# Kernel optimization log

Measured on AMD Instinct MI355X. Metric: run time of the kernel, lower is better.

Reference implementation:

```python
import jax, jax.numpy as jnp
import numpy as np


def setup_inputs() -> dict:
    key = jax.random.key(0)
    k1, k2 = jax.random.split(key)
    frame_t = jax.random.normal(k1, (8, 64, 256, 256), dtype=jnp.float32)
    # flow in pixel units (the module divides by W/H to normalize)
    flow_field = jax.random.normal(k2, (8, 2, 256, 256), dtype=jnp.float32) * 8.0
    return {"frame_t": frame_t, "flow_field": flow_field}


def _identity_grid(N, H, W, dtype):
    # F.affine_grid with identity theta, align_corners=False:
    # x_j = (2*(j+0.5))/W - 1, y_i = (2*(i+0.5))/H - 1
    xs = (jnp.arange(W, dtype=dtype) + 0.5) * (2.0 / W) - 1.0
    ys = (jnp.arange(H, dtype=dtype) + 0.5) * (2.0 / H) - 1.0
    gy, gx = jnp.meshgrid(ys, xs, indexing="ij")  # (H, W)
    grid = jnp.stack([gx, gy], axis=-1)  # (H, W, 2) with (x, y) last
    return jnp.broadcast_to(grid, (N, H, W, 2))


def _grid_sample_bilinear_zeros(img, grid):
    # img: (N, C, H, W); grid: (N, H, W, 2) normalized coords, align_corners=False,
    # padding_mode='zeros', mode='bilinear' (torch F.grid_sample defaults)
    N, C, H, W = img.shape
    x = grid[..., 0]
    y = grid[..., 1]
    # unnormalize (align_corners=False)
    ix = ((x + 1.0) * W - 1.0) * 0.5
    iy = ((y + 1.0) * H - 1.0) * 0.5
    ix0 = jnp.floor(ix)
    iy0 = jnp.floor(iy)
    ix1 = ix0 + 1.0
    iy1 = iy0 + 1.0
    wx1 = ix - ix0
    wx0 = 1.0 - wx1
    wy1 = iy - iy0
    wy0 = 1.0 - wy1

    b = jnp.arange(N)[:, None, None]  # (N,1,1)

    def gather(yy, xx):
        valid = (xx >= 0) & (xx <= W - 1) & (yy >= 0) & (yy <= H - 1)
        xc = jnp.clip(xx, 0, W - 1).astype(jnp.int32)
        yc = jnp.clip(yy, 0, H - 1).astype(jnp.int32)
        v = img[b, :, yc, xc]  # (N, H, W, C)
        return v * valid[..., None].astype(img.dtype)

    v00 = gather(iy0, ix0)
    v01 = gather(iy0, ix1)
    v10 = gather(iy1, ix0)
    v11 = gather(iy1, ix1)

    out = (v00 * (wy0 * wx0)[..., None]
           + v01 * (wy0 * wx1)[..., None]
           + v10 * (wy1 * wx0)[..., None]
           + v11 * (wy1 * wx1)[..., None])  # (N, H, W, C)
    return jnp.transpose(out, (0, 3, 1, 2))  # (N, C, H, W)


def reference(frame_t, flow_field):
    N, C, H, W = frame_t.shape
    std = _identity_grid(N, H, W, frame_t.dtype)  # (N, H, W, 2)
    # normalize flow by spatial size (channel 0 -> x/W, channel 1 -> y/H)
    scale = jnp.array([1.0 / W, 1.0 / H], dtype=flow_field.dtype).reshape(1, 2, 1, 1)
    flow_norm = flow_field * scale
    grid = std + jnp.transpose(flow_norm, (0, 2, 3, 1))  # (N, H, W, 2)
    return _grid_sample_bilinear_zeros(frame_t, grid)
```

## Files before the change

### kernel.cpp

```cpp
#include <hip/hip_runtime.h>


#define B_ 8
#define C_ 64
#define H_ 256
#define W_ 256
#define HW_ (H_ * W_)
#define BAND 16
#define NBAND (H_ / BAND)
#define HALO_LO 24
#define WROWS 64
#define WFLOATS (WROWS * W_)

__global__ __launch_bounds__(256, 2) void warp_bilinear_kernel(
    const float* __restrict__ frame,
    const float* __restrict__ flow,
    float* __restrict__ out)
{
    __shared__ float win[WFLOATS];

    const int blk  = blockIdx.x;
    const int b    = blk & 7;
    const int t    = blk >> 3;
    const int band = t & (NBAND - 1);
    const int c    = t >> 4;

    const int r0  = band * BAND;
    const int wlo = r0 - HALO_LO;

    const int tid = threadIdx.x;
    const float* __restrict__ src = frame + ((size_t)(b * C_ + c)) * HW_;

#pragma unroll
    for (int it = 0; it < WFLOATS / (256 * 4); ++it) {
        const int lin = it * 1024 + tid * 4;
        const int wr  = lin >> 8;
        const int wx  = lin & 255;
        const int gy  = min(max(wlo + wr, 0), H_ - 1);
        const float4 v = *(const float4*)(src + gy * W_ + wx);
        *(float4*)(win + lin) = v;
    }
    __syncthreads();

    const int px = tid;
    float* __restrict__ dst = out + ((size_t)(b * C_ + c)) * HW_;
    const float* __restrict__ flx = flow + (size_t)(b * 2 + 0) * HW_;
    const float* __restrict__ fly = flow + (size_t)(b * 2 + 1) * HW_;

    for (int r = 0; r < BAND; ++r) {
        const int py = r0 + r;
        const int sp = py * W_ + px;

        const float fx = flx[sp];
        const float fy = fly[sp];

        const float ix = (float)px + 0.5f * fx;
        const float iy = (float)py + 0.5f * fy;

        const float ix0f = floorf(ix);
        const float iy0f = floorf(iy);
        const float wx1 = ix - ix0f;
        const float wx0 = 1.0f - wx1;
        const float wy1 = iy - iy0f;
        const float wy0 = 1.0f - wy1;

        const int ix0 = (int)ix0f;
        const int iy0 = (int)iy0f;
        const int ix1 = ix0 + 1;
        const int iy1 = iy0 + 1;

        const float vx0 = (ix0 >= 0 && ix0 < W_) ? 1.0f : 0.0f;
        const float vx1 = (ix1 >= 0 && ix1 < W_) ? 1.0f : 0.0f;
        const float vy0 = (iy0 >= 0 && iy0 < H_) ? 1.0f : 0.0f;
        const float vy1 = (iy1 >= 0 && iy1 < H_) ? 1.0f : 0.0f;

        const int xc0 = min(max(ix0, 0), W_ - 1);
        const int xc1 = min(max(ix1, 0), W_ - 1);
        const int yc0 = min(max(iy0, 0), H_ - 1);
        const int yc1 = min(max(iy1, 0), H_ - 1);

        const float w00 = wy0 * wx0 * vy0 * vx0;
        const float w01 = wy0 * wx1 * vy0 * vx1;
        const float w10 = wy1 * wx0 * vy1 * vx0;
        const float w11 = wy1 * wx1 * vy1 * vx1;

        auto tap = [&](int yc, int xc) -> float {
            const int wr = yc - wlo;
            if ((unsigned)wr < (unsigned)WROWS) {
                return win[wr * W_ + xc];
            }
            return src[yc * W_ + xc];
        };

        const float t00 = tap(yc0, xc0);
        const float t01 = tap(yc0, xc1);
        const float t10 = tap(yc1, xc0);
        const float t11 = tap(yc1, xc1);

        const float v = w00 * t00 + w01 * t01 + w10 * t10 + w11 * t11;
        __builtin_nontemporal_store(v, dst + sp);
    }
}

extern "C" void kernel_launch(void* const* d_in, const int* in_sizes, int n_in,
                              void* d_out, int out_size, void* d_ws, size_t ws_size,
                              hipStream_t stream) {
    const float* frame = (const float*)d_in[0];
    const float* flow  = (const float*)d_in[1];
    float* out = (float*)d_out;

    dim3 grid(B_ * C_ * NBAND);
    dim3 block(256);
    warp_bilinear_kernel<<<grid, block, 0, stream>>>(frame, flow, out);
}
```

Baseline: 311.0 us.

## Process channel groups per block, reusing precomputed bilinear weights and offsets

```diff
diff --git a/kernel.cpp b/kernel.cpp
--- a/kernel.cpp
+++ b/kernel.cpp
@@ -8,97 +8,136 @@
 #define HW_ (H_ * W_)
 #define BAND 16
 #define NBAND (H_ / BAND)
-#define HALO_LO 24
-#define WROWS 64
-#define WFLOATS (WROWS * W_)
+#define CG 8
+#define NCG (C_ / CG)
+#define HALO 21
+#define WROWS 60
+#define WSTRIDE 260
+#define WFLOATS (WROWS * WSTRIDE)
 
 __global__ __launch_bounds__(256, 2) void warp_bilinear_kernel(
     const float* __restrict__ frame,
     const float* __restrict__ flow,
     float* __restrict__ out)
 {
-    __shared__ float win[WFLOATS];
+    __shared__ float winbuf[WFLOATS + 1];
+    float* win = winbuf + 1;
 
     const int blk  = blockIdx.x;
     const int b    = blk & 7;
     const int t    = blk >> 3;
     const int band = t & (NBAND - 1);
-    const int c    = t >> 4;
+    const int cg   = t >> 4;
 
     const int r0  = band * BAND;
-    const int wlo = r0 - HALO_LO;
+    const int wlo = r0 - HALO;
+    const int tid = threadIdx.x;
+    const int px  = tid;
 
-    const int tid = threadIdx.x;
-    const float* __restrict__ src = frame + ((size_t)(b * C_ + c)) * HW_;
-
-#pragma unroll
-    for (int it = 0; it < WFLOATS / (256 * 4); ++it) {
-        const int lin = it * 1024 + tid * 4;
-        const int wr  = lin >> 8;
-        const int wx  = lin & 255;
-        const int gy  = min(max(wlo + wr, 0), H_ - 1);
-        const float4 v = *(const float4*)(src + gy * W_ + wx);
-        *(float4*)(win + lin) = v;
-    }
-    __syncthreads();
-
-    const int px = tid;
-    float* __restrict__ dst = out + ((size_t)(b * C_ + c)) * HW_;
     const float* __restrict__ flx = flow + (size_t)(b * 2 + 0) * HW_;
     const float* __restrict__ fly = flow + (size_t)(b * 2 + 1) * HW_;
 
+    float w00[BAND], w01[BAND], w10[BAND], w11[BAND];
+    int   A0[BAND], A1[BAND];
+    unsigned wave_esc = 0u;
+
+#pragma unroll
     for (int r = 0; r < BAND; ++r) {
         const int py = r0 + r;
         const int sp = py * W_ + px;
-
         const float fx = flx[sp];
         const float fy = fly[sp];
-
         const float ix = (float)px + 0.5f * fx;
         const float iy = (float)py + 0.5f * fy;
-
         const float ix0f = floorf(ix);
         const float iy0f = floorf(iy);
-        const float wx1 = ix - ix0f;
-        const float wx0 = 1.0f - wx1;
-        const float wy1 = iy - iy0f;
-        const float wy0 = 1.0f - wy1;
-
+        const float tx = ix - ix0f;
+        const float ty = iy - iy0f;
         const int ix0 = (int)ix0f;
         const int iy0 = (int)iy0f;
         const int ix1 = ix0 + 1;
         const int iy1 = iy0 + 1;
-
-        const float vx0 = (ix0 >= 0 && ix0 < W_) ? 1.0f : 0.0f;
-        const float vx1 = (ix1 >= 0 && ix1 < W_) ? 1.0f : 0.0f;
-        const float vy0 = (iy0 >= 0 && iy0 < H_) ? 1.0f : 0.0f;
-        const float vy1 = (iy1 >= 0 && iy1 < H_) ? 1.0f : 0.0f;
-
-        const int xc0 = min(max(ix0, 0), W_ - 1);
-        const int xc1 = min(max(ix1, 0), W_ - 1);
+        const float vx0 = ((unsigned)ix0 < (unsigned)W_) ? 1.f : 0.f;
+        const float vx1 = ((unsigned)ix1 < (unsigned)W_) ? 1.f : 0.f;
+        const float vy0 = ((unsigned)iy0 < (unsigned)H_) ? 1.f : 0.f;
+        const float vy1 = ((unsigned)iy1 < (unsigned)H_) ? 1.f : 0.f;
+        w00[r] = (1.f - ty) * (1.f - tx) * vy0 * vx0;
+        w01[r] = (1.f - ty) * tx         * vy0 * vx1;
+        w10[r] = ty         * (1.f - tx) * vy1 * vx0;
+        w11[r] = ty         * tx         * vy1 * vx1;
         const int yc0 = min(max(iy0, 0), H_ - 1);
         const int yc1 = min(max(iy1, 0), H_ - 1);
+        const int bx  = min(max(ix0, -1), W_ - 1);
+        int wr0 = yc0 - wlo;
+        int wr1 = yc1 - wlo;
+        const bool esc = ((unsigned)wr0 >= (unsigned)WROWS) ||
+                         ((unsigned)wr1 >= (unsigned)WROWS);
+        wr0 = min(max(wr0, 0), WROWS - 1);
+        wr1 = min(max(wr1, 0), WROWS - 1);
+        A0[r] = wr0 * WSTRIDE + bx;
+        A1[r] = wr1 * WSTRIDE + bx;
+        if (__any(esc)) wave_esc |= (1u << r);
+    }
 
-        const float w00 = wy0 * wx0 * vy0 * vx0;
-        const float w01 = wy0 * wx1 * vy0 * vx1;
-        const float w10 = wy1 * wx0 * vy1 * vx0;
-        const float w11 = wy1 * wx1 * vy1 * vx1;
+    if (tid == 0) winbuf[0] = 0.f;
 
-        auto tap = [&](int yc, int xc) -> float {
-            const int wr = yc - wlo;
-            if ((unsigned)wr < (unsigned)WROWS) {
-                return win[wr * W_ + xc];
+    const size_t cbase = ((size_t)b * C_ + (size_t)cg * CG) * HW_;
+    const float* __restrict__ src0 = frame + cbase;
+    float* __restrict__ dst0 = out + cbase;
+
+    for (int cc = 0; cc < CG; ++cc) {
+        const float* __restrict__ src = src0 + (size_t)cc * HW_;
+        float* __restrict__ dst = dst0 + (size_t)cc * HW_;
+
+#pragma unroll
+        for (int it = 0; it < WROWS / 4; ++it) {
+            const int wr = it * 4 + (tid >> 6);
+            const int x4 = (tid & 63) * 4;
+            const int gy = min(max(wlo + wr, 0), H_ - 1);
+            const float4 v = *(const float4*)(src + gy * W_ + x4);
+            *(float4*)(win + wr * WSTRIDE + x4) = v;
+        }
+        if (tid < WROWS) {
+            const int gy = min(max(wlo + tid, 0), H_ - 1);
+            win[tid * WSTRIDE + 256] = src[gy * W_ + 255];
+        }
+        __syncthreads();
+
+#pragma unroll
+        for (int r = 0; r < BAND; ++r) {
+            float v = w00[r] * win[A0[r]]     + w01[r] * win[A0[r] + 1]
+                    + w10[r] * win[A1[r]]     + w11[r] * win[A1[r] + 1];
+            if (wave_esc & (1u << r)) {
+                const int py = r0 + r;
+                const int sp = py * W_ + px;
+                const float fx = flx[sp];
+                const float fy = fly[sp];
+                const float ix = (float)px + 0.5f * fx;
+                const float iy = (float)py + 0.5f * fy;
+                const float ix0f = floorf(ix);
+                const float iy0f = floorf(iy);
+                const float tx = ix - ix0f;
+                const float ty = iy - iy0f;
+                const int ix0 = (int)ix0f;
+                const int iy0 = (int)iy0f;
+                const int ix1 = ix0 + 1;
+                const int iy1 = iy0 + 1;
+                const float vx0 = ((unsigned)ix0 < (unsigned)W_) ? 1.f : 0.f;
+                const float vx1 = ((unsigned)ix1 < (unsigned)W_) ? 1.f : 0.f;
+                const float vy0 = ((unsigned)iy0 < (unsigned)H_) ? 1.f : 0.f;
+                const float vy1 = ((unsigned)iy1 < (unsigned)H_) ? 1.f : 0.f;
+                const int xc0 = min(max(ix0, 0), W_ - 1);
+                const int xc1 = min(max(ix1, 0), W_ - 1);
+                const int yc0 = min(max(iy0, 0), H_ - 1);
+                const int yc1 = min(max(iy1, 0), H_ - 1);
+                v = (1.f - ty) * (1.f - tx) * vy0 * vx0 * src[yc0 * W_ + xc0]
+                  + (1.f - ty) * tx         * vy0 * vx1 * src[yc0 * W_ + xc1]
+                  + ty         * (1.f - tx) * vy1 * vx0 * src[yc1 * W_ + xc0]
+                  + ty         * tx         * vy1 * vx1 * src[yc1 * W_ + xc1];
             }
-            return src[yc * W_ + xc];
-        };
-
-        const float t00 = tap(yc0, xc0);
-        const float t01 = tap(yc0, xc1);
-        const float t10 = tap(yc1, xc0);
-        const float t11 = tap(yc1, xc1);
-
-        const float v = w00 * t00 + w01 * t01 + w10 * t10 + w11 * t11;
-        __builtin_nontemporal_store(v, dst + sp);
+            __builtin_nontemporal_store(v, dst + (r0 + r) * W_ + px);
+        }
+        __syncthreads();
     }
 }
 
@@ -109,7 +148,7 @@
     const float* flow  = (const float*)d_in[1];
     float* out = (float*)d_out;
 
-    dim3 grid(B_ * C_ * NBAND);
+    dim3 grid(B_ * NBAND * NCG);
     dim3 block(256);
     warp_bilinear_kernel<<<grid, block, 0, stream>>>(frame, flow, out);
 }
```

After: 329.6 us. 1.06x slower.
